# Kernel optimization log

Hardware: AMD Instinct MI355X
Metric: run time of the kernel (lower is better)

The kernel has to match this reference:

```python
import jax, jax.numpy as jnp
import numpy as np

V, ENC, D, E = 10000, 2048, 512, 512
B, L = 128, 64


def setup_inputs() -> dict:
    key = jax.random.key(0)
    ks = jax.random.split(key, 12)
    s = lambda *sh: 1.0 / np.sqrt(sh[-1])
    return {
        "global_feats": jax.random.normal(ks[0], (B, ENC), jnp.float32),
        "encoded_captions": jax.random.randint(ks[1], (B, L), 0, V, jnp.int64),
        "caption_lengths": jax.random.randint(ks[2], (B,), 1, L, jnp.int64),
        "W_embed": jax.random.normal(ks[3], (V, E), jnp.float32) * 0.02,
        "W_init": jax.random.normal(ks[4], (D, ENC), jnp.float32) * s(ENC),
        "b_init": jnp.zeros((D,), jnp.float32),
        "W_ih": jax.random.normal(ks[5], (3 * D, E), jnp.float32) * s(E),
        "W_hh": jax.random.normal(ks[6], (3 * D, D), jnp.float32) * s(D),
        "b_ih": jnp.zeros((3 * D,), jnp.float32),
        "b_hh": jnp.zeros((3 * D,), jnp.float32),
        "W_fc": jax.random.normal(ks[7], (V, D), jnp.float32) * s(D),
        "b_fc": jnp.zeros((V,), jnp.float32),
    }


def reference(global_feats, encoded_captions, caption_lengths,
              W_embed, W_init, b_init, W_ih, W_hh, b_ih, b_hh, W_fc, b_fc):
    # init_hidden: h0 = tanh(Linear(global_feats))  -> (B, D)
    h0 = jnp.tanh(global_feats @ W_init.T + b_init)

    # teacher forcing over timesteps 0..L-2 (PyTorch GRU gate order: r, z, n)
    emb = W_embed[encoded_captions[:, : L - 1]]          # (B, L-1, E)
    gi = jnp.einsum('ble,ge->blg', emb, W_ih) + b_ih     # (B, L-1, 3D) precomputed input gates
    gi = jnp.swapaxes(gi, 0, 1)                          # (L-1, B, 3D) scan over time

    def step(h, gi_t):
        gh = h @ W_hh.T + b_hh                           # (B, 3D)
        i_r, i_z, i_n = jnp.split(gi_t, 3, axis=-1)
        h_r, h_z, h_n = jnp.split(gh, 3, axis=-1)
        r = jax.nn.sigmoid(i_r + h_r)
        z = jax.nn.sigmoid(i_z + h_z)
        n = jnp.tanh(i_n + r * h_n)
        h_new = (1.0 - z) * n + z * h
        return h_new, h_new

    _, hs = jax.lax.scan(step, h0, gi)                   # hs: (L-1, B, D)
    # dropout is identity in eval/reference mode
    logits = jnp.einsum('lbd,vd->blv', hs, W_fc) + b_fc  # (B, L-1, V)
    return logits, caption_lengths - 1
```

## Files before the change

### kernel.cpp

```cpp
#include <hip/hip_runtime.h>
#include <hip/hip_bf16.h>

#define V_    10000
#define ENC_  2048
#define D_    512
#define B_    128
#define L_    64
#define T_    63
#define M_    (B_ * L_ - B_)
#define G_    (3 * D_)
#define LOGITS_SZ ((long)M_ * V_)
#define SCAN_NB 64

typedef __bf16 bf16x8_t __attribute__((ext_vector_type(8)));
typedef float  f32x4_t  __attribute__((ext_vector_type(4)));
typedef short  s16x8_t  __attribute__((ext_vector_type(8)));

typedef __attribute__((address_space(3))) char*       lds_cptr_t;
typedef const __attribute__((address_space(1))) char* glb_cptr_t;

__device__ __forceinline__ void gload_lds16(const void* g, void* l) {
  __builtin_amdgcn_global_load_lds((glb_cptr_t)g, (lds_cptr_t)l, 16, 0, 0);
}
__device__ __forceinline__ float bf2f(short s) {
  return __uint_as_float(((unsigned)(unsigned short)s) << 16);
}
__device__ __forceinline__ short f2bf(float f) {
  __hip_bfloat16 h = __float2bfloat16(f);
  return *reinterpret_cast<short*>(&h);
}
__device__ __forceinline__ s16x8_t cvt8(const float* p) {
  f32x4_t lo = *reinterpret_cast<const f32x4_t*>(p);
  f32x4_t hi = *reinterpret_cast<const f32x4_t*>(p + 4);
  s16x8_t r;
#pragma unroll
  for (int e = 0; e < 4; e++) { r[e] = f2bf(lo[e]); r[4 + e] = f2bf(hi[e]); }
  return r;
}
__device__ __forceinline__ float sigmoidf_(float x) {
  return 1.0f / (1.0f + __expf(-x));
}
__device__ __forceinline__ bf16x8_t lds_frag(const short* p) {
  return __builtin_bit_cast(bf16x8_t, *reinterpret_cast<const s16x8_t*>(p));
}

__global__ void GG_cvt5(const float* __restrict__ whh, __hip_bfloat16* __restrict__ dwhh,
                        const float* __restrict__ wih, __hip_bfloat16* __restrict__ dwih,
                        const float* __restrict__ wemb, __hip_bfloat16* __restrict__ dwemb,
                        const float* __restrict__ winit, __hip_bfloat16* __restrict__ dwinit,
                        const float* __restrict__ gf, __hip_bfloat16* __restrict__ dgf) {
  const int i = blockIdx.x * blockDim.x + threadIdx.x;
  const float* s; __hip_bfloat16* d; int off;
  if (i < 98304)        { s = whh;   d = dwhh;   off = i; }
  else if (i < 196608)  { s = wih;   d = dwih;   off = i - 98304; }
  else if (i < 836608)  { s = wemb;  d = dwemb;  off = i - 196608; }
  else if (i < 967680)  { s = winit; d = dwinit; off = i - 836608; }
  else                  { s = gf;    d = dgf;    off = i - 967680; }
  s16x8_t v = cvt8(s + (long)off * 8);
  *reinterpret_cast<s16x8_t*>(d + (long)off * 8) = v;
}

__global__ void GG_cvt_kernel(const float* __restrict__ src,
                              __hip_bfloat16* __restrict__ dst, int n8) {
  int i = blockIdx.x * blockDim.x + threadIdx.x;
  if (i < n8) {
    s16x8_t v = cvt8(src + (long)i * 8);
    *reinterpret_cast<s16x8_t*>(dst + (long)i * 8) = v;
  }
}

__global__ __launch_bounds__(256) void GG_gemm_h0(
    const __hip_bfloat16* __restrict__ gfB,
    const __hip_bfloat16* __restrict__ WinitB,
    const float* __restrict__ binit,
    __hip_bfloat16* __restrict__ hfull) {
  __shared__ short sA[128 * 64];
  __shared__ short sB[128 * 64];
  const int lane = threadIdx.x & 63;
  const int wave = threadIdx.x >> 6;
  const int n0 = blockIdx.x * 128;
  const int srow = lane >> 3;
  const int scol = (lane & 7) * 8;

  f32x4_t acc[4][4] = {};

  const __hip_bfloat16* aptr[4];
  const __hip_bfloat16* bptr[4];
#pragma unroll
  for (int i = 0; i < 4; i++) {
    const int r = (wave * 4 + i) * 8 + srow;
    aptr[i] = gfB + (long)r * ENC_ + scol;
    bptr[i] = WinitB + (long)(n0 + r) * ENC_ + scol;
  }

  const int wm = (wave >> 1) * 64;
  const int wn = (wave & 1) * 64;
  const int fr = lane & 15;
  const int fk = (lane >> 4) * 8;

  for (int kt = 0; kt < 32; kt++) {
    __syncthreads();
#pragma unroll
    for (int i = 0; i < 4; i++) {
      const int chunk = wave * 4 + i;
      gload_lds16(aptr[i] + kt * 64, sA + chunk * 512);
      gload_lds16(bptr[i] + kt * 64, sB + chunk * 512);
    }
    __syncthreads();
#pragma unroll
    for (int kk = 0; kk < 2; kk++) {
      bf16x8_t a[4], b[4];
#pragma unroll
      for (int i = 0; i < 4; i++) {
        a[i] = lds_frag(sA + (wm + i * 16 + fr) * 64 + kk * 32 + fk);
        b[i] = lds_frag(sB + (wn + i * 16 + fr) * 64 + kk * 32 + fk);
      }
#pragma unroll
      for (int i = 0; i < 4; i++)
#pragma unroll
        for (int j = 0; j < 4; j++)
          acc[i][j] = __builtin_amdgcn_mfma_f32_16x16x32_bf16(a[i], b[j], acc[i][j], 0, 0, 0);
    }
  }

  const int fq = lane >> 4;
#pragma unroll
  for (int j = 0; j < 4; j++) {
    const int n = n0 + wn + j * 16 + fr;
    const float bv = binit[n];
#pragma unroll
    for (int i = 0; i < 4; i++)
#pragma unroll
      for (int rr = 0; rr < 4; rr++) {
        const int m = wm + i * 16 + fq * 4 + rr;
        hfull[(long)m * 64 * 512 + n] = __float2bfloat16(tanhf(acc[i][j][rr] + bv));
      }
  }
}

__global__ __launch_bounds__(256) void GG_gemm_gi(
    const __hip_bfloat16* __restrict__ WembB,
    const int* __restrict__ cap,
    const __hip_bfloat16* __restrict__ WihB,
    const float* __restrict__ bias,
    __hip_bfloat16* __restrict__ C) {
  __shared__ short sA[128 * 64];
  __shared__ short sB[128 * 64];
  const int lane = threadIdx.x & 63;
  const int wave = threadIdx.x >> 6;
  const int m0 = blockIdx.y * 128;
  const int n0 = blockIdx.x * 128;
  const int srow = lane >> 3;
  const int scol = (lane & 7) * 8;

  f32x4_t acc[4][4] = {};

  const __hip_bfloat16* aptr[4];
  const __hip_bfloat16* bptr[4];
#pragma unroll
  for (int i = 0; i < 4; i++) {
    const int r = (wave * 4 + i) * 8 + srow;
    const int bt = m0 + r;
    const int bb = bt / 63;
    const int tt = bt - bb * 63;
    aptr[i] = WembB + (long)cap[bb * L_ + tt] * 512 + scol;
    bptr[i] = WihB + (long)(n0 + r) * 512 + scol;
  }

  const int wm = (wave >> 1) * 64;
  const int wn = (wave & 1) * 64;
  const int fr = lane & 15;
  const int fk = (lane >> 4) * 8;

  for (int kt = 0; kt < 8; kt++) {
    __syncthreads();
#pragma unroll
    for (int i = 0; i < 4; i++) {
      const int chunk = wave * 4 + i;
      gload_lds16(aptr[i] + kt * 64, sA + chunk * 512);
      gload_lds16(bptr[i] + kt * 64, sB + chunk * 512);
    }
    __syncthreads();
#pragma unroll
    for (int kk = 0; kk < 2; kk++) {
      bf16x8_t a[4], b[4];
#pragma unroll
      for (int i = 0; i < 4; i++) {
        a[i] = lds_frag(sA + (wm + i * 16 + fr) * 64 + kk * 32 + fk);
        b[i] = lds_frag(sB + (wn + i * 16 + fr) * 64 + kk * 32 + fk);
      }
#pragma unroll
      for (int i = 0; i < 4; i++)
#pragma unroll
        for (int j = 0; j < 4; j++)
          acc[i][j] = __builtin_amdgcn_mfma_f32_16x16x32_bf16(a[i], b[j], acc[i][j], 0, 0, 0);
    }
  }

  const int fq = lane >> 4;
#pragma unroll
  for (int j = 0; j < 4; j++) {
    const int n = n0 + wn + j * 16 + fr;
    const float bv = bias[n];
#pragma unroll
    for (int i = 0; i < 4; i++)
#pragma unroll
      for (int rr = 0; rr < 4; rr++) {
        const int m = m0 + wm + i * 16 + fq * 4 + rr;
        C[(long)m * G_ + n] = __float2bfloat16(acc[i][j][rr] + bv);
      }
  }
}

template <bool BBF16>
__global__ __launch_bounds__(256) void GG_gemm_logits(
    const __hip_bfloat16* __restrict__ hfull,
    const void* __restrict__ Bsrc,
    const float* __restrict__ bias,
    float* __restrict__ C) {
  const int flat = blockIdx.x;
  const int xcd = flat & 7;
  const int s = flat >> 3;
  const int col = xcd * 10 + s % 10;
  const int row = s / 10;
  if (col >= 79) return;
  const int m0 = row * 128;
  const int n0 = col * 128;

  __shared__ short sA[128 * 64];
  __shared__ short sB[128 * 64];
  const int lane = threadIdx.x & 63;
  const int wave = threadIdx.x >> 6;
  const int srow = lane >> 3;
  const int scol = (lane & 7) * 8;

  f32x4_t acc[4][4] = {};

  const __hip_bfloat16* aptr[4];
  const __hip_bfloat16* bptrB[4];
  const float* bptrF[4];
#pragma unroll
  for (int i = 0; i < 4; i++) {
    const int r = (wave * 4 + i) * 8 + srow;
    const int m = m0 + r;
    const int bb = m / 63;
    const int tt = m - bb * 63;
    aptr[i] = hfull + ((long)bb * 64 + tt + 1) * 512 + scol;
    int nrow = n0 + r;
    nrow = (nrow < V_) ? nrow : (V_ - 1);
    if constexpr (BBF16) bptrB[i] = (const __hip_bfloat16*)Bsrc + (long)nrow * 512 + scol;
    else                 bptrF[i] = (const float*)Bsrc + (long)nrow * 512 + scol;
  }

  const int wm = (wave >> 1) * 64;
  const int wn = (wave & 1) * 64;
  const int fr = lane & 15;
  const int fk = (lane >> 4) * 8;

  for (int kt = 0; kt < 8; kt++) {
    s16x8_t vb[4];
    if constexpr (!BBF16) {
#pragma unroll
      for (int i = 0; i < 4; i++) vb[i] = cvt8(bptrF[i] + kt * 64);
    }
    __syncthreads();
#pragma unroll
    for (int i = 0; i < 4; i++) {
      const int chunk = wave * 4 + i;
      gload_lds16(aptr[i] + kt * 64, sA + chunk * 512);
      if constexpr (BBF16)
        gload_lds16(bptrB[i] + kt * 64, sB + chunk * 512);
      else
        *reinterpret_cast<s16x8_t*>(sB + chunk * 512 + lane * 8) = vb[i];
    }
    __syncthreads();
#pragma unroll
    for (int kk = 0; kk < 2; kk++) {
      bf16x8_t a[4], b[4];
#pragma unroll
      for (int i = 0; i < 4; i++) {
        a[i] = lds_frag(sA + (wm + i * 16 + fr) * 64 + kk * 32 + fk);
        b[i] = lds_frag(sB + (wn + i * 16 + fr) * 64 + kk * 32 + fk);
      }
#pragma unroll
      for (int i = 0; i < 4; i++)
#pragma unroll
        for (int j = 0; j < 4; j++)
          acc[i][j] = __builtin_amdgcn_mfma_f32_16x16x32_bf16(a[i], b[j], acc[i][j], 0, 0, 0);
    }
  }

  const int fq = lane >> 4;
#pragma unroll
  for (int j = 0; j < 4; j++) {
    const int n = n0 + wn + j * 16 + fr;
    if (n >= V_) continue;
    const float bv = bias[n];
#pragma unroll
    for (int i = 0; i < 4; i++)
#pragma unroll
      for (int rr = 0; rr < 4; rr++) {
        const int m = m0 + wm + i * 16 + fq * 4 + rr;
        C[(long)m * V_ + n] = acc[i][j][rr] + bv;
      }
  }
}

__global__ __launch_bounds__(256) void GG_scan_persist(
    __hip_bfloat16* __restrict__ hfull,
    const __hip_bfloat16* __restrict__ gi,
    const __hip_bfloat16* __restrict__ WhhB,
    const float* __restrict__ bhh,
    int* __restrict__ flagbase) {
  __shared__ short sW[48 * 512];
  __shared__ short sA[4][16 * 512];
  const int lane = threadIdx.x & 63;
  const int wave = threadIdx.x >> 6;
  const int strip = blockIdx.x & 31;
  const int half  = blockIdx.x >> 5;
  const int d0 = strip * 16;
  const int fr = lane & 15;
  const int g4 = lane >> 4;
  int* myflags = flagbase + half * 32;

  for (int rr = wave; rr < 48; rr += 4) {
    const int grow = (rr >> 4) * 512 + d0 + (rr & 15);
    gload_lds16(WhhB + (long)grow * 512 + (lane ^ (rr & 7)) * 8, sW + rr * 512);
  }

  const int dd = d0 + fr;
  const int bbase = half * 64 + wave * 16 + g4 * 4;
  const float br_ = bhh[dd], bz_ = bhh[512 + dd], bn_ = bhh[1024 + dd];
  const short* gis = (const short*)gi;
  short* sAw = &sA[wave][0];

  float hp[4];
#pragma unroll
  for (int rr = 0; rr < 4; rr++)
    hp[rr] = bf2f(*(const short*)&hfull[((long)(bbase + rr) * 64) * 512 + dd]);

  asm volatile("s_waitcnt vmcnt(0)" ::: "memory");
  __syncthreads();

  for (int t = 0; t < T_; t++) {
    short gir[4], giz[4], gin[4];
#pragma unroll
    for (int rr = 0; rr < 4; rr++) {
      const long gbase = ((long)(bbase + rr) * T_ + t) * (long)G_;
      gir[rr] = gis[gbase + dd];
      giz[rr] = gis[gbase + 512 + dd];
      gin[rr] = gis[gbase + 1024 + dd];
    }

    if (t > 0) {
      if (threadIdx.x < 64) {
        while (true) {
          int v = t;
          if (lane < 32)
            v = __hip_atomic_load(&myflags[lane], __ATOMIC_ACQUIRE,
                                  __HIP_MEMORY_SCOPE_AGENT);
          if (__all(v >= t)) break;
          __builtin_amdgcn_s_sleep(4);
        }
      }
      __syncthreads();
    }

#pragma unroll
    for (int r = 0; r < 16; r++) {
      const int b = half * 64 + wave * 16 + r;
      gload_lds16(hfull + ((long)b * 64 + t) * 512 + (lane ^ (r & 7)) * 8,
                  sAw + r * 512);
    }
    asm volatile("s_waitcnt vmcnt(0)" ::: "memory");
    __builtin_amdgcn_sched_barrier(0);

    f32x4_t acc[3] = {};
#pragma unroll
    for (int kt = 0; kt < 8; kt++)
#pragma unroll
      for (int kk = 0; kk < 2; kk++) {
        const int kg = kt * 8 + kk * 4 + g4;
        const int gsw = (kg ^ (fr & 7)) * 8;
        bf16x8_t afr = lds_frag(sAw + fr * 512 + gsw);
        bf16x8_t bfr[3];
#pragma unroll
        for (int j = 0; j < 3; j++) bfr[j] = lds_frag(sW + (j * 16 + fr) * 512 + gsw);
#pragma unroll
        for (int j = 0; j < 3; j++)
          acc[j] = __builtin_amdgcn_mfma_f32_16x16x32_bf16(afr, bfr[j], acc[j], 0, 0, 0);
      }

#pragma unroll
    for (int rr = 0; rr < 4; rr++) {
      const float rg = sigmoidf_(bf2f(gir[rr]) + acc[0][rr] + br_);
      const float zg = sigmoidf_(bf2f(giz[rr]) + acc[1][rr] + bz_);
      const float ng = tanhf(bf2f(gin[rr]) + rg * (acc[2][rr] + bn_));
      const short hnb = f2bf((1.f - zg) * ng + zg * hp[rr]);
      hp[rr] = bf2f(hnb);
      *(short*)&hfull[((long)(bbase + rr) * 64 + t + 1) * 512 + dd] = hnb;
    }

    if (t < T_ - 1) {
      __syncthreads();
      if (threadIdx.x == 0)
        __hip_atomic_store(&myflags[strip], t + 1, __ATOMIC_RELEASE,
                           __HIP_MEMORY_SCOPE_AGENT);
    }
  }
}

__global__ void GG_tail_kernel(const int* __restrict__ lens, float* __restrict__ out) {
  const int b = threadIdx.x;
  if (b < B_) out[LOGITS_SZ + b] = (float)(lens[b] - 1);
}

extern "C" void kernel_launch(void* const* d_in, const int* in_sizes, int n_in,
                              void* d_out, int out_size, void* d_ws, size_t ws_size,
                              hipStream_t stream) {
  const float* gf      = (const float*)d_in[0];
  const int*   cap     = (const int*)d_in[1];
  const int*   lens    = (const int*)d_in[2];
  const float* W_embed = (const float*)d_in[3];
  const float* W_init  = (const float*)d_in[4];
  const float* b_init  = (const float*)d_in[5];
  const float* W_ih    = (const float*)d_in[6];
  const float* W_hh    = (const float*)d_in[7];
  const float* b_ih    = (const float*)d_in[8];
  const float* b_hh    = (const float*)d_in[9];
  const float* W_fc    = (const float*)d_in[10];
  const float* b_fc    = (const float*)d_in[11];
  float* out = (float*)d_out;

  char* ob = (char*)d_out;
  __hip_bfloat16* gi_ws  = (__hip_bfloat16*)ob;
  __hip_bfloat16* WhhB   = (__hip_bfloat16*)(ob + 25165824);
  __hip_bfloat16* WihB   = (__hip_bfloat16*)(ob + 27262976);
  __hip_bfloat16* WembB  = (__hip_bfloat16*)(ob + 29360128);
  __hip_bfloat16* WinitB = (__hip_bfloat16*)(ob + 40894464);
  __hip_bfloat16* gfB    = (__hip_bfloat16*)(ob + 43253760);

  __hip_bfloat16* hfull = (__hip_bfloat16*)d_ws;
  __hip_bfloat16* WfcB  = (__hip_bfloat16*)((char*)d_ws + 8388608);
  const bool big_ws = ws_size >= (size_t)(8388608 + 10240000 + 256);
  int* flags = (int*)((char*)d_ws + (big_ws ? 18628608 : 8388608));

  hipMemsetAsync(flags, 0, 256, stream);

  GG_cvt5<<<dim3(3908), 256, 0, stream>>>(W_hh, WhhB, W_ih, WihB, W_embed, WembB,
                                          W_init, WinitB, gf, gfB);
  if (big_ws)
    GG_cvt_kernel<<<dim3((V_ * D_ / 8 + 255) / 256), 256, 0, stream>>>(W_fc, WfcB, V_ * D_ / 8);

  GG_gemm_h0<<<dim3(4), 256, 0, stream>>>(gfB, WinitB, b_init, hfull);

  GG_gemm_gi<<<dim3(G_ / 128, M_ / 128), 256, 0, stream>>>(WembB, cap, WihB, b_ih, gi_ws);

  GG_scan_persist<<<dim3(SCAN_NB), 256, 0, stream>>>(hfull, gi_ws, WhhB, b_hh, flags);

  if (big_ws)
    GG_gemm_logits<true><<<dim3(5040), 256, 0, stream>>>(hfull, WfcB, b_fc, out);
  else
    GG_gemm_logits<false><<<dim3(5040), 256, 0, stream>>>(hfull, W_fc, b_fc, out);

  GG_tail_kernel<<<dim3(1), 128, 0, stream>>>(lens, out);
}
```

Baseline: 590.0 us.

## Load scan hidden-state fragments directly into registers with coherent loads, relax flag ordering

The persistent GRU scan kernel no longer stages the per-step hidden-state tile through LDS. Each lane now issues sixteen global_load_dwordx4 with sc0 sc1 (cache-bypassing) straight into MFMA A-fragment registers, and the new hidden values are written back with sc0 sc1 global_store_short. Cross-block flags switch from acquire/release atomics to relaxed system-scope atomics with a shorter sleep, relying on the explicit cache bits and a vmcnt wait before the barrier for visibility. This targets per-step latency and memory-fence cost on the serial critical path. The trade-off is more VGPR pressure, and correctness now depends on hand-placed cache-coherence bits instead of formal memory ordering.

```diff
diff --git a/kernel.cpp b/kernel.cpp
--- a/kernel.cpp
+++ b/kernel.cpp
@@ -313,7 +313,6 @@
     const float* __restrict__ bhh,
     int* __restrict__ flagbase) {
   __shared__ short sW[48 * 512];
-  __shared__ short sA[4][16 * 512];
   const int lane = threadIdx.x & 63;
   const int wave = threadIdx.x >> 6;
   const int strip = blockIdx.x & 31;
@@ -332,7 +331,16 @@
   const int bbase = half * 64 + wave * 16 + g4 * 4;
   const float br_ = bhh[dd], bz_ = bhh[512 + dd], bn_ = bhh[1024 + dd];
   const short* gis = (const short*)gi;
-  short* sAw = &sA[wave][0];
+
+  const int arow = half * 64 + wave * 16 + fr;
+  const unsigned long long abase0 =
+      (unsigned long long)hfull + ((unsigned long long)arow * 64 * 512 + (unsigned)(g4 * 8)) * 2ull;
+
+  unsigned long long sbase[4];
+#pragma unroll
+  for (int rr = 0; rr < 4; rr++)
+    sbase[rr] = (unsigned long long)hfull +
+                ((unsigned long long)(bbase + rr) * 64 * 512 + (unsigned)dd) * 2ull;
 
   float hp[4];
 #pragma unroll
@@ -357,39 +365,40 @@
         while (true) {
           int v = t;
           if (lane < 32)
-            v = __hip_atomic_load(&myflags[lane], __ATOMIC_ACQUIRE,
-                                  __HIP_MEMORY_SCOPE_AGENT);
+            v = __hip_atomic_load(&myflags[lane], __ATOMIC_RELAXED,
+                                  __HIP_MEMORY_SCOPE_SYSTEM);
           if (__all(v >= t)) break;
-          __builtin_amdgcn_s_sleep(4);
+          __builtin_amdgcn_s_sleep(1);
         }
       }
       __syncthreads();
     }
 
-#pragma unroll
-    for (int r = 0; r < 16; r++) {
-      const int b = half * 64 + wave * 16 + r;
-      gload_lds16(hfull + ((long)b * 64 + t) * 512 + (lane ^ (r & 7)) * 8,
-                  sAw + r * 512);
-    }
+    const unsigned long long ab = abase0 + (unsigned long long)t * 1024ull;
+    f32x4_t a[16];
+#define ALOAD(IDX, OFF)                                                        \
+    asm volatile("global_load_dwordx4 %0, %1, off offset:" #OFF " sc0 sc1"     \
+                 : "=v"(a[IDX]) : "v"(ab));
+    ALOAD(0, 0)    ALOAD(1, 64)   ALOAD(2, 128)  ALOAD(3, 192)
+    ALOAD(4, 256)  ALOAD(5, 320)  ALOAD(6, 384)  ALOAD(7, 448)
+    ALOAD(8, 512)  ALOAD(9, 576)  ALOAD(10, 640) ALOAD(11, 704)
+    ALOAD(12, 768) ALOAD(13, 832) ALOAD(14, 896) ALOAD(15, 960)
+#undef ALOAD
     asm volatile("s_waitcnt vmcnt(0)" ::: "memory");
     __builtin_amdgcn_sched_barrier(0);
 
     f32x4_t acc[3] = {};
 #pragma unroll
-    for (int kt = 0; kt < 8; kt++)
-#pragma unroll
-      for (int kk = 0; kk < 2; kk++) {
-        const int kg = kt * 8 + kk * 4 + g4;
-        const int gsw = (kg ^ (fr & 7)) * 8;
-        bf16x8_t afr = lds_frag(sAw + fr * 512 + gsw);
-        bf16x8_t bfr[3];
-#pragma unroll
-        for (int j = 0; j < 3; j++) bfr[j] = lds_frag(sW + (j * 16 + fr) * 512 + gsw);
-#pragma unroll
-        for (int j = 0; j < 3; j++)
-          acc[j] = __builtin_amdgcn_mfma_f32_16x16x32_bf16(afr, bfr[j], acc[j], 0, 0, 0);
-      }
+    for (int kt = 0; kt < 16; kt++) {
+      const bf16x8_t afr = __builtin_bit_cast(bf16x8_t, a[kt]);
+      const int gsw = ((kt * 4 + g4) ^ (fr & 7)) * 8;
+      bf16x8_t bfr[3];
+#pragma unroll
+      for (int j = 0; j < 3; j++) bfr[j] = lds_frag(sW + (j * 16 + fr) * 512 + gsw);
+#pragma unroll
+      for (int j = 0; j < 3; j++)
+        acc[j] = __builtin_amdgcn_mfma_f32_16x16x32_bf16(afr, bfr[j], acc[j], 0, 0, 0);
+    }
 
 #pragma unroll
     for (int rr = 0; rr < 4; rr++) {
@@ -398,14 +407,18 @@
       const float ng = tanhf(bf2f(gin[rr]) + rg * (acc[2][rr] + bn_));
       const short hnb = f2bf((1.f - zg) * ng + zg * hp[rr]);
       hp[rr] = bf2f(hnb);
-      *(short*)&hfull[((long)(bbase + rr) * 64 + t + 1) * 512 + dd] = hnb;
+      const unsigned long long saddr = sbase[rr] + (unsigned long long)(t + 1) * 1024ull;
+      const unsigned int val = (unsigned short)hnb;
+      asm volatile("global_store_short %0, %1, off sc0 sc1"
+                   :: "v"(saddr), "v"(val) : "memory");
     }
 
     if (t < T_ - 1) {
+      asm volatile("s_waitcnt vmcnt(0)" ::: "memory");
       __syncthreads();
       if (threadIdx.x == 0)
-        __hip_atomic_store(&myflags[strip], t + 1, __ATOMIC_RELEASE,
-                           __HIP_MEMORY_SCOPE_AGENT);
+        __hip_atomic_store(&myflags[strip], t + 1, __ATOMIC_RELAXED,
+                           __HIP_MEMORY_SCOPE_SYSTEM);
     }
   }
 }
```

After: 587.6 us. About the same (-0.4%).
